# Performance work log

Measured on AMD Instinct MI355X. Metric: run time of the kernel, lower is better.

Reference implementation:

```python
import jax, jax.numpy as jnp
import numpy as np
import math

E = 8192        # number of hyperedges in the batch
IN_DIM = 256
OUT_DIM = 128


def setup_inputs() -> dict:
    key = jax.random.key(0)
    k1, k2, k3, k4 = jax.random.split(key, 4)
    node_embeddings = jax.random.normal(k1, (E, IN_DIM), dtype=jnp.float32)
    # xavier_uniform-like scale for the projection weights
    lim = 1.414 * math.sqrt(6.0 / (IN_DIM + OUT_DIM))
    query_weight = jax.random.uniform(k2, (IN_DIM, OUT_DIM), minval=-lim, maxval=lim, dtype=jnp.float32)
    key_weight = jax.random.uniform(k3, (IN_DIM, OUT_DIM), minval=-lim, maxval=lim, dtype=jnp.float32)
    # binary hypergraph connectivity mask [E, E]; diagonal forced to 1 so no row is fully masked
    mask = jax.random.randint(k4, (E, E), 0, 2, dtype=jnp.int32)
    mask = mask.at[jnp.arange(E), jnp.arange(E)].set(1)
    return {
        "node_embeddings": node_embeddings,
        "query_weight": query_weight,
        "key_weight": key_weight,
        "attention_mask": mask,
    }


def reference(node_embeddings, query_weight, key_weight, attention_mask):
    # QK projections: [E, in] x [in, out] -> [E, out]
    q = node_embeddings @ query_weight
    k = node_embeddings @ key_weight
    # scaled scores [E, E]
    scores = (q @ k.T) / jnp.sqrt(jnp.asarray(OUT_DIM, dtype=q.dtype))
    # masked_fill(mask == 0, -inf)
    scores = jnp.where(attention_mask == 0, jnp.asarray(-jnp.inf, dtype=scores.dtype), scores)
    probs = jax.nn.softmax(scores, axis=1)
    # output aggregates the KEY projections (as in the original code)
    return probs @ k
```

## Files before the change

### kernel.cpp

```cpp
#include <hip/hip_runtime.h>
#include <stdint.h>

#define E_N 8192
#define SPLIT 4
#define CH 32
#define QBLK 64

typedef unsigned short u16;
typedef unsigned int u32;
typedef unsigned long long u64;
typedef __attribute__((ext_vector_type(4))) float f32x4;
typedef __attribute__((ext_vector_type(8))) short bf16x8;
typedef __attribute__((ext_vector_type(4))) unsigned int u32x4;
typedef __attribute__((ext_vector_type(2))) unsigned int u32x2;

union V16 { u32x4 q; bf16x8 h; u16 u[8]; };

static __device__ __forceinline__ u16 f2bf(float f) {
  union { float f; unsigned u; } c; c.f = f;
  unsigned r = c.u + 0x7FFFu + ((c.u >> 16) & 1u);
  return (u16)(r >> 16);
}

constexpr float QS = 1.4426950408889634f / 11.313708498984761f;

__global__ void k_wt(const float* __restrict__ Wq, const float* __restrict__ Wk,
                     u16* __restrict__ wt) {
  int idx = blockIdx.x * 256 + threadIdx.x;
  int mat = idx >> 15, rem = idx & 32767;
  float v = mat ? Wk[rem] : Wq[rem];
  int d = rem >> 7, c = rem & 127;
  wt[(mat * 128 + c) * 256 + d] = f2bf(v);
}

__launch_bounds__(256)
__global__ void k_proj(const float* __restrict__ X, const u16* __restrict__ wt,
                       u16* __restrict__ qg, u16* __restrict__ kg) {
  __shared__ __align__(16) char Xs[64 * 512];
  const int tid = threadIdx.x;
  const int wid = tid >> 6, lane = tid & 63, g = lane >> 4, l15 = lane & 15;
  const int r0 = blockIdx.x * 64;
#pragma unroll
  for (int i = 0; i < 16; ++i) {
    int s = tid + 256 * i;
    int row = s >> 6, c4 = (s & 63) << 2;
    f32x4 v = *(const f32x4*)(X + (size_t)(r0 + row) * 256 + c4);
    u32x2 pk;
    pk[0] = f2bf(v[0]) | ((unsigned)f2bf(v[1]) << 16);
    pk[1] = f2bf(v[2]) | ((unsigned)f2bf(v[3]) << 16);
    *(u32x2*)(Xs + (((row << 9) + (c4 << 1)) ^ ((row & 7) << 4))) = pk;
  }
  __syncthreads();
  bf16x8 xa[8];
  const int arow = wid * 16 + l15;
#pragma unroll
  for (int ks = 0; ks < 8; ++ks) {
    V16 t; t.q = *(const u32x4*)(Xs + (((arow << 9) + (ks << 6) + (g << 4)) ^ ((l15 & 7) << 4)));
    xa[ks] = t.h;
  }
  const f32x4 zero4 = {0.f, 0.f, 0.f, 0.f};
  f32x4 acc[16];
#pragma unroll
  for (int i = 0; i < 16; ++i) acc[i] = zero4;
#pragma unroll
  for (int ct = 0; ct < 16; ++ct) {
    int mat = ct >> 3, c = ((ct & 7) << 4) + l15;
#pragma unroll
    for (int ks = 0; ks < 8; ++ks) {
      V16 b; b.q = *(const u32x4*)(wt + ((mat * 128 + c) * 256 + (ks << 5) + (g << 3)));
      acc[ct] = __builtin_amdgcn_mfma_f32_16x16x32_bf16(xa[ks], b.h, acc[ct], 0, 0, 0);
    }
  }
#pragma unroll
  for (int ct = 0; ct < 16; ++ct) {
    int mat = ct >> 3, c = ((ct & 7) << 4) + l15;
#pragma unroll
    for (int r = 0; r < 4; ++r) {
      int row = r0 + wid * 16 + 4 * g + r;
      float v = acc[ct][r];
      if (mat == 0) qg[row * 128 + c] = f2bf(v * QS);
      else          kg[row * 128 + c] = f2bf(v);
    }
  }
}

__global__ void k_kt(const u16* __restrict__ kg, u16* __restrict__ ktg) {
  __shared__ __align__(16) u16 Ts[64 * 66];
  const int tid = threadIdx.x;
  const int b = blockIdx.x;
  const int r0 = (b >> 1) * 64, c0 = (b & 1) * 64;
#pragma unroll
  for (int i = 0; i < 2; ++i) {
    int s = tid + 256 * i;
    int row = s >> 3, seg = s & 7;
    u32x4 v = *(const u32x4*)(kg + (size_t)(r0 + row) * 128 + c0 + seg * 8);
    unsigned* dst = (unsigned*)((char*)Ts + row * 132 + seg * 16);
    dst[0] = v[0]; dst[1] = v[1]; dst[2] = v[2]; dst[3] = v[3];
  }
  __syncthreads();
#pragma unroll
  for (int i = 0; i < 2; ++i) {
    int s = tid + 256 * i;
    int oc = s >> 3, seg2 = s & 7;
    u16 t[8];
#pragma unroll
    for (int j = 0; j < 8; ++j) t[j] = Ts[(seg2 * 8 + j) * 66 + oc];
    u32x4 o;
    o[0] = t[0] | ((unsigned)t[1] << 16);
    o[1] = t[2] | ((unsigned)t[3] << 16);
    o[2] = t[4] | ((unsigned)t[5] << 16);
    o[3] = t[6] | ((unsigned)t[7] << 16);
    *(u32x4*)(ktg + (size_t)(c0 + oc) * E_N + r0 + seg2 * 8) = o;
  }
}

#define BARRIER() { asm volatile("s_waitcnt lgkmcnt(0)" ::: "memory"); \
                    __builtin_amdgcn_s_barrier(); }

#define LOADREGS(KV1)                                                           \
  {                                                                             \
    const u16* kp = kgp + (size_t)(KV1) * 128;                                  \
    kr0 = *(const u32x4*)(kp);                                                  \
    kr1 = *(const u32x4*)(kp + 16 * 128);                                       \
    kr2 = *(const u32x4*)(kp + 32 * 128);                                       \
    kr3 = *(const u32x4*)(kp + 48 * 128);                                       \
    const u16* tp = ktp + (KV1);                                                \
    tr0 = *(const u32x4*)(tp);                                                  \
    tr1 = *(const u32x4*)(tp + 32 * E_N);                                       \
    tr2 = *(const u32x4*)(tp + 64 * E_N);                                       \
    tr3 = *(const u32x4*)(tp + 96 * E_N);                                       \
  }

#define WRITELDS(KW, TW)                                                        \
  {                                                                             \
    *(u32x4*)((KW) + kofs)          = kr0;                                      \
    *(u32x4*)((KW) + kofs + 4096)   = kr1;                                      \
    *(u32x4*)((KW) + kofs + 8192)   = kr2;                                      \
    *(u32x4*)((KW) + kofs + 12288)  = kr3;                                      \
    *(u32x4*)((TW) + tofs)          = tr0;                                      \
    *(u32x4*)((TW) + tofs + 4096)   = tr1;                                      \
    *(u32x4*)((TW) + tofs + 8192)   = tr2;                                      \
    *(u32x4*)((TW) + tofs + 12288)  = tr3;                                      \
  }

#define MASKLOAD(SET, KV1)                                                      \
  {                                                                             \
    _Pragma("unroll")                                                           \
    for (int t4 = 0; t4 < 4; ++t4)                                              \
      SET[t4] = *(const u32x4*)(mrow + (KV1) + t4 * 16);                        \
  }

#define FSTEP(SUB, KR, TR, KW, TW, MSET, DOM, DOP, DOW)                         \
  {                                                                             \
    f32x4 S[4];                                                                 \
    _Pragma("unroll")                                                           \
    for (int t = 0; t < 4; ++t) S[t] = zero4;                                   \
    __builtin_amdgcn_s_setprio(1);                                              \
    _Pragma("unroll")                                                           \
    for (int t = 0; t < 4; ++t) {                                               \
      int krow = t * 16 + l15;                                                  \
      _Pragma("unroll")                                                         \
      for (int ks = 0; ks < 4; ++ks) {                                          \
        V16 kf; kf.q = *(const u32x4*)((KR) + (((krow << 8) + (ks << 6) + (g << 4)) ^ ((l15 & 7) << 4))); \
        S[t] = __builtin_amdgcn_mfma_f32_16x16x32_bf16(kf.h, qf[ks], S[t], 0, 0, 0); \
      }                                                                         \
    }                                                                           \
    __builtin_amdgcn_s_setprio(0);                                              \
    _Pragma("unroll")                                                           \
    for (int t = 0; t < 4; ++t) {                                               \
      float p0 = MSET[t][0] ? __builtin_amdgcn_exp2f(S[t][0]) : 0.f;            \
      float p1 = MSET[t][1] ? __builtin_amdgcn_exp2f(S[t][1]) : 0.f;            \
      float p2 = MSET[t][2] ? __builtin_amdgcn_exp2f(S[t][2]) : 0.f;            \
      float p3 = MSET[t][3] ? __builtin_amdgcn_exp2f(S[t][3]) : 0.f;            \
      lacc += (p0 + p1) + (p2 + p3);                                            \
      u32x2 pk;                                                                 \
      pk[0] = f2bf(p0) | ((u32)f2bf(p1) << 16);                                 \
      pk[1] = f2bf(p2) | ((u32)f2bf(p3) << 16);                                 \
      *(u32x2*)(Pw + ((l15 * 128 + (t * 16 + 4 * g) * 2) ^ ((l15 & 7) << 4))) = pk; \
    }                                                                           \
    if (DOM) {                                                                  \
      MASKLOAD(mqa, kvbase + (((st2 + 2 + qb) & (CH - 1)) << 6))                \
      MASKLOAD(mqb, kvbase + (((st2 + 3 + qb) & (CH - 1)) << 6))                \
    }                                                                           \
    bf16x8 pa0, pa1;                                                            \
    { V16 t2; t2.q = *(const u32x4*)(Pw + ((l15 * 128 + g * 16) ^ ((l15 & 7) << 4))); pa0 = t2.h; } \
    { V16 t2; t2.q = *(const u32x4*)(Pw + ((l15 * 128 + 64 + g * 16) ^ ((l15 & 7) << 4))); pa1 = t2.h; } \
    __builtin_amdgcn_s_setprio(1);                                              \
    _Pragma("unroll")                                                           \
    for (int dt = 0; dt < 8; ++dt) {                                            \
      int krow = dt * 16 + l15;                                                 \
      V16 kf0; kf0.q = *(const u32x4*)((TR) + (((krow << 7) + (g << 4)) ^ ((l15 & 7) << 4))); \
      Oacc[dt] = __builtin_amdgcn_mfma_f32_16x16x32_bf16(pa0, kf0.h, Oacc[dt], 0, 0, 0); \
      V16 kf1; kf1.q = *(const u32x4*)((TR) + (((krow << 7) + 64 + (g << 4)) ^ ((l15 & 7) << 4))); \
      Oacc[dt] = __builtin_amdgcn_mfma_f32_16x16x32_bf16(pa1, kf1.h, Oacc[dt], 0, 0, 0); \
    }                                                                           \
    __builtin_amdgcn_s_setprio(0);                                              \
    if (DOW) WRITELDS(KW, TW)                                                   \
    if (DOP) {                                                                  \
      const int kvt = kvbase + (((st2 + (SUB) + 2 + qb) & (CH - 1)) << 6);      \
      LOADREGS(kvt)                                                             \
    }                                                                           \
    if (DOW) BARRIER()                                                          \
  }

__launch_bounds__(256, 2)
__global__ void k_flash(const u16* __restrict__ qg, const u16* __restrict__ kg,
                        const u16* __restrict__ ktg, const int* __restrict__ M,
                        float* __restrict__ Op, float* __restrict__ lp) {
  __shared__ __align__(16) char K0[64 * 256], K1[64 * 256];
  __shared__ __align__(16) char T0[128 * 128], T1[128 * 128];
  __shared__ __align__(16) char Psh[4 * 2048];
  const int tid = threadIdx.x;
  const int wid = tid >> 6, lane = tid & 63, g = lane >> 4, l15 = lane & 15;
  const int bid = blockIdx.x;
  const int split = bid & (SPLIT - 1), qb = bid >> 2;
  const int qb0 = qb * QBLK;
  const int kvbase = split * (E_N / SPLIT);
  char* Pw = Psh + wid * 2048;
  const u32* mrow = (const u32*)M + (size_t)(qb0 + wid * 16 + l15) * E_N + 4 * g;
  u32x4 mqa[4], mqb[4];

  const int kr_r = tid >> 4, kr_s = tid & 15;
  const int tr_d = tid >> 3, tr_s = tid & 7;
  const int kofs = ((kr_r << 8) + (kr_s << 4)) ^ ((kr_r & 7) << 4);
  const int tofs = ((tr_d << 7) + (tr_s << 4)) ^ ((tr_d & 7) << 4);
  const u16* kgp = kg + (size_t)kr_r * 128 + kr_s * 8;
  const u16* ktp = ktg + (size_t)tr_d * E_N + tr_s * 8;
  u32x4 kr0, kr1, kr2, kr3, tr0, tr1, tr2, tr3;

  bf16x8 qf[4];
  {
    const u16* qrow = qg + (size_t)(qb0 + wid * 16 + l15) * 128;
#pragma unroll
    for (int ks = 0; ks < 4; ++ks) {
      V16 t; t.q = *(const u32x4*)(qrow + (ks << 5) + (g << 3));
      qf[ks] = t.h;
    }
  }
  const f32x4 zero4 = {0.f, 0.f, 0.f, 0.f};
  f32x4 Oacc[8];
#pragma unroll
  for (int i = 0; i < 8; ++i) Oacc[i] = zero4;
  float lacc = 0.f;

  {
    const int c0 = (qb & (CH - 1)) << 6;
    const int c1 = ((qb + 1) & (CH - 1)) << 6;
    MASKLOAD(mqa, kvbase + c0)
    MASKLOAD(mqb, kvbase + c1)
    LOADREGS(kvbase + c0)
    WRITELDS(K0, T0)
    LOADREGS(kvbase + c1)
    BARRIER()
  }

  for (int st2 = 0; st2 < CH; st2 += 2) {
    FSTEP(0, K0, T0, K1, T1, mqa, false, (st2 < CH - 2), true)
    FSTEP(1, K1, T1, K0, T0, mqb, (st2 < CH - 2), (st2 < CH - 2), (st2 < CH - 2))
  }

  {
    float v = lacc;
    v += __shfl_xor(v, 16);
    v += __shfl_xor(v, 32);
    if (lane < 16)
      lp[split * E_N + qb0 + wid * 16 + lane] = v;
  }
  float* op = Op + ((size_t)split * E_N + qb0 + wid * 16) * 128;
#pragma unroll
  for (int dt = 0; dt < 8; ++dt)
#pragma unroll
    for (int r = 0; r < 4; ++r)
      op[(4 * g + r) * 128 + dt * 16 + l15] = Oacc[dt][r];
}

__global__ void k_comb(const float* __restrict__ Op, const float* __restrict__ lp,
                       float* __restrict__ out) {
  int idx4 = blockIdx.x * 256 + threadIdx.x;
  int base = idx4 << 2;
  int e = base >> 7;
  f32x4 o = {0.f, 0.f, 0.f, 0.f};
  float l = 0.f;
#pragma unroll
  for (int s = 0; s < SPLIT; ++s) {
    o += *(const f32x4*)(Op + (size_t)s * (E_N * 128) + base);
    l += lp[s * E_N + e];
  }
  float rl = 1.0f / l;
  o[0] *= rl; o[1] *= rl; o[2] *= rl; o[3] *= rl;
  *(f32x4*)(out + base) = o;
}

extern "C" void kernel_launch(void* const* d_in, const int* in_sizes, int n_in,
                              void* d_out, int out_size, void* d_ws, size_t ws_size,
                              hipStream_t stream) {
  const float* X  = (const float*)d_in[0];
  const float* Wq = (const float*)d_in[1];
  const float* Wk = (const float*)d_in[2];
  const int*   M  = (const int*)d_in[3];
  char* ws = (char*)d_ws;
  u16*   qg   = (u16*)(ws);
  u16*   kg   = (u16*)(ws + (size_t)(2u << 20));
  u16*   ktg  = (u16*)(ws + (size_t)(4u << 20));
  u16*   wt   = (u16*)(ws + (size_t)(6u << 20));
  float* lp   = (float*)(ws + (size_t)(6u << 20) + (128u << 10));
  float* Op   = (float*)(ws + (size_t)(6u << 20) + (512u << 10) + (8u << 20));
  float* out = (float*)d_out;

  k_wt  <<<256, 256, 0, stream>>>(Wq, Wk, wt);
  k_proj<<<128, 256, 0, stream>>>(X, wt, qg, kg);
  k_kt  <<<256, 256, 0, stream>>>(kg, ktg);
  k_flash<<<SPLIT * (E_N / QBLK), 256, 0, stream>>>(qg, kg, ktg, M, Op, lp);
  k_comb<<<(E_N * 128 / 4) / 256, 256, 0, stream>>>(Op, lp, out);
}
```

Measured before the change: 115.5 us.

## Read transposed K operand from global directly and double the KV split

The PV stage no longer stages the transposed K tile in LDS. Each wave now loads its MFMA B fragments straight from global memory inside the dt loop, which removes the T0/T1 buffers, their LDS writes and the priority hints around that MFMA loop. SPLIT goes from 4 to 8 with half as many chunks per block, so there are twice as many blocks with shorter KV ranges. In exchange, the four waves fetch the same data redundantly through the cache, global-load latency sits unprefetched inside the MFMA loop, and the combine step has more partial results to merge.

```diff
diff --git a/kernel.cpp b/kernel.cpp
--- a/kernel.cpp
+++ b/kernel.cpp
@@ -2,8 +2,8 @@
 #include <stdint.h>
 
 #define E_N 8192
-#define SPLIT 4
-#define CH 32
+#define SPLIT 8
+#define CH 16
 #define QBLK 64
 
 typedef unsigned short u16;
@@ -124,23 +124,14 @@
     kr1 = *(const u32x4*)(kp + 16 * 128);                                       \
     kr2 = *(const u32x4*)(kp + 32 * 128);                                       \
     kr3 = *(const u32x4*)(kp + 48 * 128);                                       \
-    const u16* tp = ktp + (KV1);                                                \
-    tr0 = *(const u32x4*)(tp);                                                  \
-    tr1 = *(const u32x4*)(tp + 32 * E_N);                                       \
-    tr2 = *(const u32x4*)(tp + 64 * E_N);                                       \
-    tr3 = *(const u32x4*)(tp + 96 * E_N);                                       \
-  }
-
-#define WRITELDS(KW, TW)                                                        \
+  }
+
+#define WRITELDS(KW)                                                            \
   {                                                                             \
     *(u32x4*)((KW) + kofs)          = kr0;                                      \
     *(u32x4*)((KW) + kofs + 4096)   = kr1;                                      \
     *(u32x4*)((KW) + kofs + 8192)   = kr2;                                      \
     *(u32x4*)((KW) + kofs + 12288)  = kr3;                                      \
-    *(u32x4*)((TW) + tofs)          = tr0;                                      \
-    *(u32x4*)((TW) + tofs + 4096)   = tr1;                                      \
-    *(u32x4*)((TW) + tofs + 8192)   = tr2;                                      \
-    *(u32x4*)((TW) + tofs + 12288)  = tr3;                                      \
   }
 
 #define MASKLOAD(SET, KV1)                                                      \
@@ -150,8 +141,9 @@
       SET[t4] = *(const u32x4*)(mrow + (KV1) + t4 * 16);                        \
   }
 
-#define FSTEP(SUB, KR, TR, KW, TW, MSET, DOM, DOP, DOW)                         \
+#define FSTEP(SUB, KR, KW, MSET, DOM, DOP, DOW)                                 \
   {                                                                             \
+    const int cur = kvbase + (((st2 + (SUB) + qb) & (CH - 1)) << 6);            \
     f32x4 S[4];                                                                 \
     _Pragma("unroll")                                                           \
     for (int t = 0; t < 4; ++t) S[t] = zero4;                                   \
@@ -185,17 +177,15 @@
     bf16x8 pa0, pa1;                                                            \
     { V16 t2; t2.q = *(const u32x4*)(Pw + ((l15 * 128 + g * 16) ^ ((l15 & 7) << 4))); pa0 = t2.h; } \
     { V16 t2; t2.q = *(const u32x4*)(Pw + ((l15 * 128 + 64 + g * 16) ^ ((l15 & 7) << 4))); pa1 = t2.h; } \
-    __builtin_amdgcn_s_setprio(1);                                              \
     _Pragma("unroll")                                                           \
     for (int dt = 0; dt < 8; ++dt) {                                            \
-      int krow = dt * 16 + l15;                                                 \
-      V16 kf0; kf0.q = *(const u32x4*)((TR) + (((krow << 7) + (g << 4)) ^ ((l15 & 7) << 4))); \
+      const u16* kp2 = ktp2 + (size_t)(dt * 16) * E_N + cur;                    \
+      V16 kf0; kf0.q = *(const u32x4*)(kp2);                                    \
       Oacc[dt] = __builtin_amdgcn_mfma_f32_16x16x32_bf16(pa0, kf0.h, Oacc[dt], 0, 0, 0); \
-      V16 kf1; kf1.q = *(const u32x4*)((TR) + (((krow << 7) + 64 + (g << 4)) ^ ((l15 & 7) << 4))); \
+      V16 kf1; kf1.q = *(const u32x4*)(kp2 + 32);                               \
       Oacc[dt] = __builtin_amdgcn_mfma_f32_16x16x32_bf16(pa1, kf1.h, Oacc[dt], 0, 0, 0); \
     }                                                                           \
-    __builtin_amdgcn_s_setprio(0);                                              \
-    if (DOW) WRITELDS(KW, TW)                                                   \
+    if (DOW) WRITELDS(KW)                                                       \
     if (DOP) {                                                                  \
       const int kvt = kvbase + (((st2 + (SUB) + 2 + qb) & (CH - 1)) << 6);      \
       LOADREGS(kvt)                                                             \
@@ -208,12 +198,11 @@
                         const u16* __restrict__ ktg, const int* __restrict__ M,
                         float* __restrict__ Op, float* __restrict__ lp) {
   __shared__ __align__(16) char K0[64 * 256], K1[64 * 256];
-  __shared__ __align__(16) char T0[128 * 128], T1[128 * 128];
   __shared__ __align__(16) char Psh[4 * 2048];
   const int tid = threadIdx.x;
   const int wid = tid >> 6, lane = tid & 63, g = lane >> 4, l15 = lane & 15;
   const int bid = blockIdx.x;
-  const int split = bid & (SPLIT - 1), qb = bid >> 2;
+  const int split = bid & (SPLIT - 1), qb = bid >> 3;
   const int qb0 = qb * QBLK;
   const int kvbase = split * (E_N / SPLIT);
   char* Pw = Psh + wid * 2048;
@@ -221,12 +210,10 @@
   u32x4 mqa[4], mqb[4];
 
   const int kr_r = tid >> 4, kr_s = tid & 15;
-  const int tr_d = tid >> 3, tr_s = tid & 7;
   const int kofs = ((kr_r << 8) + (kr_s << 4)) ^ ((kr_r & 7) << 4);
-  const int tofs = ((tr_d << 7) + (tr_s << 4)) ^ ((tr_d & 7) << 4);
   const u16* kgp = kg + (size_t)kr_r * 128 + kr_s * 8;
-  const u16* ktp = ktg + (size_t)tr_d * E_N + tr_s * 8;
-  u32x4 kr0, kr1, kr2, kr3, tr0, tr1, tr2, tr3;
+  const u16* ktp2 = ktg + (size_t)l15 * E_N + 8 * g;
+  u32x4 kr0, kr1, kr2, kr3;
 
   bf16x8 qf[4];
   {
@@ -249,14 +236,14 @@
     MASKLOAD(mqa, kvbase + c0)
     MASKLOAD(mqb, kvbase + c1)
     LOADREGS(kvbase + c0)
-    WRITELDS(K0, T0)
+    WRITELDS(K0)
     LOADREGS(kvbase + c1)
     BARRIER()
   }
 
   for (int st2 = 0; st2 < CH; st2 += 2) {
-    FSTEP(0, K0, T0, K1, T1, mqa, false, (st2 < CH - 2), true)
-    FSTEP(1, K1, T1, K0, T0, mqb, (st2 < CH - 2), (st2 < CH - 2), (st2 < CH - 2))
+    FSTEP(0, K0, K1, mqa, false, (st2 < CH - 2), true)
+    FSTEP(1, K1, K0, mqb, (st2 < CH - 2), (st2 < CH - 2), (st2 < CH - 2))
   }
 
   {
```

Measured after the change: 216.0 us. 1.87x slower.
